# Performance work log

Hardware: AMD Instinct MI355X
Metric: run time of the kernel (lower is better)

The kernel has to match this reference:

```python
import jax, jax.numpy as jnp
import numpy as np

B, N, C = 4, 2048, 1024
H = 16
D = C // H  # head_dim = 64
EPS = 1e-5


def layer_norm(x, g, b):
    mu = jnp.mean(x, axis=-1, keepdims=True)
    var = jnp.var(x, axis=-1, keepdims=True)
    return (x - mu) * jax.lax.rsqrt(var + EPS) * g + b


def setup_inputs() -> dict:
    key = jax.random.key(0)
    ks = jax.random.split(key, 12)
    s = 0.02
    return {
        "x": jax.random.normal(ks[0], (B, N, C), dtype=jnp.float32),
        "Wqkv": jax.random.normal(ks[1], (C, 3 * C), dtype=jnp.float32) * s,
        "bqkv": jnp.zeros((3 * C,), dtype=jnp.float32),
        "Wproj": jax.random.normal(ks[2], (C, C), dtype=jnp.float32) * s,
        "bproj": jnp.zeros((C,), dtype=jnp.float32),
        "g1": jnp.ones((C,), dtype=jnp.float32),
        "b1": jnp.zeros((C,), dtype=jnp.float32),
        "g2": jnp.ones((C,), dtype=jnp.float32),
        "b2": jnp.zeros((C,), dtype=jnp.float32),
        "W1": jax.random.normal(ks[3], (C, 4 * C), dtype=jnp.float32) * s,
        "bf1": jnp.zeros((4 * C,), dtype=jnp.float32),
        "W2": jax.random.normal(ks[4], (4 * C, C), dtype=jnp.float32) * s,
        "bf2": jnp.zeros((C,), dtype=jnp.float32),
    }


def reference(x, Wqkv, bqkv, Wproj, bproj, g1, b1, g2, b2, W1, bf1, W2, bf2):
    # Pre-norm MHA (dropout = identity in eval mode)
    shortcut = x
    h = layer_norm(x, g1, b1)
    qkv = h @ Wqkv + bqkv                       # [B,N,3C]
    qkv = qkv.reshape(B, N, 3, H, D)
    q = jnp.transpose(qkv[:, :, 0], (0, 2, 1, 3))  # [B,H,N,D]
    k = jnp.transpose(qkv[:, :, 1], (0, 2, 1, 3))
    v = jnp.transpose(qkv[:, :, 2], (0, 2, 1, 3))
    scale = D ** -0.5
    attn = jnp.einsum("bhqd,bhkd->bhqk", q, k) * scale
    attn = jax.nn.softmax(attn, axis=-1)
    o = jnp.einsum("bhqk,bhkd->bhqd", attn, v)  # [B,H,N,D]
    o = jnp.transpose(o, (0, 2, 1, 3)).reshape(B, N, C)
    x = o @ Wproj + bproj + shortcut
    # FFN with exact GELU (torch nn.GELU default)
    h2 = layer_norm(x, g2, b2)
    ffn = jax.nn.gelu(h2 @ W1 + bf1, approximate=False) @ W2 + bf2
    return x + ffn
```

## Files before the change

kernel.cpp:

```cpp
#include <hip/hip_runtime.h>
#include <math.h>

using u16 = unsigned short;
typedef __bf16 bf16x8 __attribute__((ext_vector_type(8)));
typedef float f32x4 __attribute__((ext_vector_type(4)));
typedef short s16x4 __attribute__((ext_vector_type(4)));

__device__ __forceinline__ float b2f(u16 u) {
    union { unsigned u; float f; } c; c.u = ((unsigned)u) << 16; return c.f;
}
__device__ __forceinline__ u16 f2b(float f) {
    union { float f; unsigned u; } c; c.f = f;
    return (u16)((c.u + 0x7fffu + ((c.u >> 16) & 1u)) >> 16);
}
__device__ __forceinline__ u16 chop(float f) {
    union { float f; unsigned u; } c; c.f = f;
    return (u16)(c.u >> 16);
}

struct F8 { float v[8]; };
__device__ __forceinline__ F8 unpack8(uint4 r) {
    F8 o;
    o.v[0] = b2f((u16)r.x); o.v[1] = b2f((u16)(r.x >> 16));
    o.v[2] = b2f((u16)r.y); o.v[3] = b2f((u16)(r.y >> 16));
    o.v[4] = b2f((u16)r.z); o.v[5] = b2f((u16)(r.z >> 16));
    o.v[6] = b2f((u16)r.w); o.v[7] = b2f((u16)(r.w >> 16));
    return o;
}

__device__ __forceinline__ void gll16(const void* g, void* l) {
    __builtin_amdgcn_global_load_lds((const __attribute__((address_space(1))) void*)g,
                                     (__attribute__((address_space(3))) void*)l, 16, 0, 0);
}

__global__ __launch_bounds__(256)
void prep_k(const void* __restrict__ s0, const void* __restrict__ s1,
            const void* __restrict__ s2, const void* __restrict__ s3,
            const void* __restrict__ s4, const void* __restrict__ s5,
            const void* __restrict__ s6, const void* __restrict__ s7,
            u16* __restrict__ vec, int* __restrict__ flagp) {
    const u16* gp = (const u16*)s2;
    const int flag = (gp[0] == 0x3F80 && gp[1] == 0x3F80) ? 0 : 1;
    const int i = blockIdx.x * 256 + threadIdx.x;
    if (i == 0) *flagp = flag;
    const void* src; int off;
    if      (i < 3072)  { src = s0; off = 0; }
    else if (i < 4096)  { src = s1; off = 3072; }
    else if (i < 5120)  { src = s2; off = 4096; }
    else if (i < 6144)  { src = s3; off = 5120; }
    else if (i < 7168)  { src = s4; off = 6144; }
    else if (i < 8192)  { src = s5; off = 7168; }
    else if (i < 12288) { src = s6; off = 8192; }
    else                { src = s7; off = 12288; }
    const int j = i - off;
    vec[i] = flag ? f2b(((const float*)src)[j]) : ((const u16*)src)[j];
}

__global__ __launch_bounds__(256)
void transpose_k(const void* __restrict__ src, u16* __restrict__ dst,
                 int R, int Cc, int srcStride, int srcOff, const int* __restrict__ flagp) {
    const int flag = *flagp;
    __shared__ u16 t[32][33];
    const int bx = blockIdx.x * 32;
    const int by = blockIdx.y * 32;
    const int tx = threadIdx.x & 31;
    const int ty = threadIdx.x >> 5;
    if (flag) {
        const float* s = (const float*)src + srcOff;
#pragma unroll
        for (int i = 0; i < 32; i += 8)
            t[ty + i][tx] = f2b(s[(size_t)(by + ty + i) * srcStride + bx + tx]);
    } else {
        const u16* s = (const u16*)src + srcOff;
#pragma unroll
        for (int i = 0; i < 32; i += 8)
            t[ty + i][tx] = s[(size_t)(by + ty + i) * srcStride + bx + tx];
    }
    __syncthreads();
#pragma unroll
    for (int i = 0; i < 32; i += 8)
        dst[(size_t)(bx + ty + i) * R + by + tx] = t[tx][ty + i];
}

__global__ __launch_bounds__(256)
void ln_kernel(const void* __restrict__ x, const u16* __restrict__ g,
               const u16* __restrict__ b, u16* __restrict__ out,
               int srcExt, const int* __restrict__ flagp) {
    const int eff = srcExt ? *flagp : 0;
    const int row = blockIdx.x;
    const int tid = threadIdx.x;
    float v0, v1, v2, v3;
    if (eff) {
        const float4 f = *(const float4*)((const float*)x + (size_t)row * 1024 + tid * 4);
        v0 = f.x; v1 = f.y; v2 = f.z; v3 = f.w;
    } else {
        const uint2 raw = *(const uint2*)((const u16*)x + (size_t)row * 1024 + tid * 4);
        v0 = b2f((u16)raw.x); v1 = b2f((u16)(raw.x >> 16));
        v2 = b2f((u16)raw.y); v3 = b2f((u16)(raw.y >> 16));
    }
    float s  = v0 + v1 + v2 + v3;
    float ss = v0 * v0 + v1 * v1 + v2 * v2 + v3 * v3;
#pragma unroll
    for (int off = 32; off > 0; off >>= 1) {
        s  += __shfl_down(s,  off, 64);
        ss += __shfl_down(ss, off, 64);
    }
    __shared__ float red[8];
    const int wave = tid >> 6, lane = tid & 63;
    if (lane == 0) { red[wave] = s; red[4 + wave] = ss; }
    __syncthreads();
    s  = red[0] + red[1] + red[2] + red[3];
    ss = red[4] + red[5] + red[6] + red[7];
    const float mu  = s * (1.f / 1024.f);
    const float var = ss * (1.f / 1024.f) - mu * mu;
    const float rs  = rsqrtf(var + 1e-5f);
    const int c = tid * 4;
    const uint2 graw = *(const uint2*)(g + c);
    const uint2 braw = *(const uint2*)(b + c);
    u16 o0 = f2b((v0 - mu) * rs * b2f((u16)graw.x)         + b2f((u16)braw.x));
    u16 o1 = f2b((v1 - mu) * rs * b2f((u16)(graw.x >> 16)) + b2f((u16)(braw.x >> 16)));
    u16 o2 = f2b((v2 - mu) * rs * b2f((u16)graw.y)         + b2f((u16)braw.y));
    u16 o3 = f2b((v3 - mu) * rs * b2f((u16)(graw.y >> 16)) + b2f((u16)(braw.y >> 16)));
    uint2 w; w.x = (unsigned)o0 | ((unsigned)o1 << 16); w.y = (unsigned)o2 | ((unsigned)o3 << 16);
    *(uint2*)(out + (size_t)row * 1024 + c) = w;
}

template<int ACT, bool ACCUM, bool RES_EXT>
__global__ __launch_bounds__(256)
void gemm_bt(const u16* __restrict__ A, const u16* __restrict__ Bt,
             const u16* __restrict__ bias, const void* __restrict__ res,
             u16* __restrict__ C, int M, int K, int ldc, const int* __restrict__ flagp) {
    const int flag = RES_EXT ? *flagp : 0;
    __shared__ u16 As[128 * 32];
    __shared__ u16 Bs[128 * 32];
    const int tid  = threadIdx.x;
    const int lane = tid & 63;
    const int wave = tid >> 6;
    const int wr   = (wave >> 1) * 64;
    const int wc   = (wave & 1) * 64;
    const int lr   = lane & 15;
    const int quad = lane >> 4;
    const int bm = blockIdx.x * 128;
    const int bn = blockIdx.y * 128;
    const int scol = (tid & 3) * 8;
    const int srow = tid >> 2;

    f32x4 acc[4][4] = {};

    const u16* Arow0 = A  + (size_t)(bm + srow) * K + scol;
    const u16* Arow1 = A  + (size_t)(bm + 64 + srow) * K + scol;
    const u16* Brow0 = Bt + (size_t)(bn + srow) * K + scol;
    const u16* Brow1 = Bt + (size_t)(bn + 64 + srow) * K + scol;

    u16* asd0 = &As[wave * 512];
    u16* asd1 = &As[2048 + wave * 512];
    u16* bsd0 = &Bs[wave * 512];
    u16* bsd1 = &Bs[2048 + wave * 512];

    for (int k0 = 0; k0 < K; k0 += 32) {
        gll16(Arow0 + k0, asd0);
        gll16(Arow1 + k0, asd1);
        gll16(Brow0 + k0, bsd0);
        gll16(Brow1 + k0, bsd1);
        __syncthreads();
        bf16x8 af[4], bfr[4];
#pragma unroll
        for (int i = 0; i < 4; ++i)
            af[i] = *(const bf16x8*)(&As[(wr + i * 16 + lr) * 32 + quad * 8]);
#pragma unroll
        for (int j = 0; j < 4; ++j)
            bfr[j] = *(const bf16x8*)(&Bs[(wc + j * 16 + lr) * 32 + quad * 8]);
#pragma unroll
        for (int i = 0; i < 4; ++i)
#pragma unroll
            for (int j = 0; j < 4; ++j)
                acc[i][j] = __builtin_amdgcn_mfma_f32_16x16x32_bf16(af[i], bfr[j], acc[i][j], 0, 0, 0);
        __syncthreads();
    }

#pragma unroll
    for (int i = 0; i < 4; ++i) {
#pragma unroll
        for (int j = 0; j < 4; ++j) {
#pragma unroll
            for (int r = 0; r < 4; ++r) {
                const int row = bm + wr + i * 16 + quad * 4 + r;
                const int col = bn + wc + j * 16 + lr;
                const size_t idx = (size_t)row * ldc + col;
                float v = acc[i][j][r];
                if (bias) v += b2f(bias[col]);
                if (ACT == 1) v = 0.5f * v * (1.0f + erff(v * 0.70710678118654752f));
                if (res) {
                    if (RES_EXT && flag) v += ((const float*)res)[idx];
                    else                 v += b2f(((const u16*)res)[idx]);
                }
                if (ACCUM) v += b2f(C[idx]);
                C[idx] = f2b(v);
            }
        }
    }
}

__device__ __forceinline__ void stage4(const u16* __restrict__ A,
        const u16* __restrict__ Bt, char* lds, int bm, int bn, int K,
        int t, int ty, int tid) {
    const int k0   = t << 6;
    const int bufo = (t & 1) << 16;
    const u16* src;
    int rowbase, base;
    if (ty < 2) { src = A;  rowbase = bm + ty * 128;       base = bufo + ty * 16384; }
    else        { src = Bt; rowbase = bn + (ty - 2) * 128; base = bufo + 32768 + (ty - 2) * 16384; }
#pragma unroll
    for (int i = 0; i < 2; ++i) {
        const int w    = tid * 16 + i * 8192;
        const int row  = w >> 7;
        const int colB = (w & 127) ^ ((row & 7) << 4);
        const u16* g = src + (size_t)(rowbase + row) * K + k0 + (colB >> 1);
        char* d = lds + base + ((tid >> 6) << 10) + i * 8192;
        gll16(g, d);
    }
}
__device__ __forceinline__ void stage3(const u16* __restrict__ A,
        const u16* __restrict__ Bt, char* lds, int bm, int bn, int K,
        int t, int ty, int tid) {
    const int k0   = t << 6;
    const int bufo = (t & 1) * 49152;
    const u16* src;
    int rowbase, base;
    if (ty < 2) { src = A;  rowbase = bm + ty * 128; base = bufo + ty * 16384; }
    else        { src = Bt; rowbase = bn;            base = bufo + 32768; }
#pragma unroll
    for (int i = 0; i < 2; ++i) {
        const int w    = tid * 16 + i * 8192;
        const int row  = w >> 7;
        const int colB = (w & 127) ^ ((row & 7) << 4);
        const u16* g = src + (size_t)(rowbase + row) * K + k0 + (colB >> 1);
        char* d = lds + base + ((tid >> 6) << 10) + i * 8192;
        gll16(g, d);
    }
}

template<int ACT, bool RES_EXT>
__global__ __launch_bounds__(512, 2)
void gemm256(const u16* __restrict__ A, const u16* __restrict__ Bt,
             const u16* __restrict__ bias, const void* __restrict__ res,
             u16* __restrict__ C, int nbx, int K, int ldc,
             const int* __restrict__ flagp) {
    extern __shared__ char lds[];
    const int flag = RES_EXT ? *flagp : 0;

    const int nwg = gridDim.x;
    const int q8  = nwg >> 3;
    const int bid = blockIdx.x;
    const int swz = (bid & 7) * q8 + (bid >> 3);
    const int bm  = (swz % nbx) * 256;
    const int bn  = (swz / nbx) * 256;

    const int tid  = threadIdx.x;
    const int lane = tid & 63, wave = tid >> 6;
    const int lr   = lane & 15, quad = lane >> 4;
    const int wm   = wave >> 2, wn = wave & 3;

    const int nt    = K >> 6;
    const int niter = nt >> 1;

    stage4(A, Bt, lds, bm, bn, K, 0, 0, tid);
    stage4(A, Bt, lds, bm, bn, K, 0, 2, tid);
    stage4(A, Bt, lds, bm, bn, K, 0, 1, tid);
    stage4(A, Bt, lds, bm, bn, K, 0, 3, tid);
    stage4(A, Bt, lds, bm, bn, K, 1, 0, tid);
    stage4(A, Bt, lds, bm, bn, K, 1, 2, tid);
    stage4(A, Bt, lds, bm, bn, K, 1, 1, tid);
    asm volatile("s_waitcnt vmcnt(6)" ::: "memory");
    __builtin_amdgcn_s_barrier();

    f32x4 acc[8][4] = {};
    const int cq = quad * 16;

    for (int it = 0; it < niter; ++it) {
        const bool lastpair = (it == niter - 1);
#pragma unroll
        for (int hf = 0; hf < 2; ++hf) {
            const int T    = 2 * it + hf;
            const int bufo = (T & 1) << 16;
            bf16x8 a0[4][2], a1[4][2], b0[2][2], b1[2][2];

#pragma unroll
            for (int m = 0; m < 4; ++m) {
                const int rA = wm * 64 + m * 16 + lr;
                const int sw = (rA & 7) << 4;
#pragma unroll
                for (int ks = 0; ks < 2; ++ks)
                    a0[m][ks] = *(const bf16x8*)(lds + bufo + rA * 128 + ((ks * 64 + cq) ^ sw));
            }
#pragma unroll
            for (int n = 0; n < 2; ++n) {
                const int rB = wn * 32 + n * 16 + lr;
                const int sw = (rB & 7) << 4;
#pragma unroll
                for (int ks = 0; ks < 2; ++ks)
                    b0[n][ks] = *(const bf16x8*)(lds + bufo + 32768 + rB * 128 + ((ks * 64 + cq) ^ sw));
            }
            if (T + 1 < nt) stage4(A, Bt, lds, bm, bn, K, T + 1, 3, tid);
            __builtin_amdgcn_s_barrier();
            asm volatile("s_waitcnt lgkmcnt(0)" ::: "memory");
            __builtin_amdgcn_s_setprio(1);
#pragma unroll
            for (int m = 0; m < 4; ++m)
#pragma unroll
                for (int n = 0; n < 2; ++n) {
                    acc[m][n] = __builtin_amdgcn_mfma_f32_16x16x32_bf16(a0[m][0], b0[n][0], acc[m][n], 0, 0, 0);
                    acc[m][n] = __builtin_amdgcn_mfma_f32_16x16x32_bf16(a0[m][1], b0[n][1], acc[m][n], 0, 0, 0);
                }
            __builtin_amdgcn_s_setprio(0);
            __builtin_amdgcn_s_barrier();

#pragma unroll
            for (int n = 0; n < 2; ++n) {
                const int rB = wn * 32 + n * 16 + lr;
                const int sw = (rB & 7) << 4;
#pragma unroll
                for (int ks = 0; ks < 2; ++ks)
                    b1[n][ks] = *(const bf16x8*)(lds + bufo + 49152 + rB * 128 + ((ks * 64 + cq) ^ sw));
            }
            if (T + 2 < nt) stage4(A, Bt, lds, bm, bn, K, T + 2, 0, tid);
            __builtin_amdgcn_s_barrier();
            asm volatile("s_waitcnt lgkmcnt(0)" ::: "memory");
            __builtin_amdgcn_s_setprio(1);
#pragma unroll
            for (int m = 0; m < 4; ++m)
#pragma unroll
                for (int n = 0; n < 2; ++n) {
                    acc[m][2 + n] = __builtin_amdgcn_mfma_f32_16x16x32_bf16(a0[m][0], b1[n][0], acc[m][2 + n], 0, 0, 0);
                    acc[m][2 + n] = __builtin_amdgcn_mfma_f32_16x16x32_bf16(a0[m][1], b1[n][1], acc[m][2 + n], 0, 0, 0);
                }
            __builtin_amdgcn_s_setprio(0);
            __builtin_amdgcn_s_barrier();

#pragma unroll
            for (int m = 0; m < 4; ++m) {
                const int rA = wm * 64 + m * 16 + lr;
                const int sw = (rA & 7) << 4;
#pragma unroll
                for (int ks = 0; ks < 2; ++ks)
                    a1[m][ks] = *(const bf16x8*)(lds + bufo + 16384 + rA * 128 + ((ks * 64 + cq) ^ sw));
            }
            if (T + 2 < nt) stage4(A, Bt, lds, bm, bn, K, T + 2, 2, tid);
            __builtin_amdgcn_s_barrier();
            asm volatile("s_waitcnt lgkmcnt(0)" ::: "memory");
            __builtin_amdgcn_s_setprio(1);
#pragma unroll
            for (int m = 0; m < 4; ++m)
#pragma unroll
                for (int n = 0; n < 2; ++n) {
                    acc[4 + m][n] = __builtin_amdgcn_mfma_f32_16x16x32_bf16(a1[m][0], b0[n][0], acc[4 + m][n], 0, 0, 0);
                    acc[4 + m][n] = __builtin_amdgcn_mfma_f32_16x16x32_bf16(a1[m][1], b0[n][1], acc[4 + m][n], 0, 0, 0);
                }
            __builtin_amdgcn_s_setprio(0);
            __builtin_amdgcn_s_barrier();

            if (T + 2 < nt) stage4(A, Bt, lds, bm, bn, K, T + 2, 1, tid);
            if (lastpair) asm volatile("s_waitcnt vmcnt(0)" ::: "memory");
            else          asm volatile("s_waitcnt vmcnt(6)" ::: "memory");
            __builtin_amdgcn_s_barrier();
            __builtin_amdgcn_s_setprio(1);
#pragma unroll
            for (int m = 0; m < 4; ++m)
#pragma unroll
                for (int n = 0; n < 2; ++n) {
                    acc[4 + m][2 + n] = __builtin_amdgcn_mfma_f32_16x16x32_bf16(a1[m][0], b1[n][0], acc[4 + m][2 + n], 0, 0, 0);
                    acc[4 + m][2 + n] = __builtin_amdgcn_mfma_f32_16x16x32_bf16(a1[m][1], b1[n][1], acc[4 + m][2 + n], 0, 0, 0);
                }
            __builtin_amdgcn_s_setprio(0);
            __builtin_amdgcn_s_barrier();
        }
    }

#pragma unroll
    for (int mi = 0; mi < 8; ++mi) {
        const int row = bm + (mi >> 2) * 128 + wm * 64 + (mi & 3) * 16 + quad * 4;
#pragma unroll
        for (int nj = 0; nj < 4; ++nj) {
            const int col = bn + (nj >> 1) * 128 + wn * 32 + (nj & 1) * 16 + lr;
            const float bia = bias ? b2f(bias[col]) : 0.f;
#pragma unroll
            for (int r = 0; r < 4; ++r) {
                const size_t idx = (size_t)(row + r) * ldc + col;
                float v = acc[mi][nj][r] + bia;
                if (ACT == 1) v = 0.5f * v * (1.0f + erff(v * 0.70710678118654752f));
                if (res) {
                    if (RES_EXT && flag) v += ((const float*)res)[idx];
                    else                 v += b2f(((const u16*)res)[idx]);
                }
                C[idx] = f2b(v);
            }
        }
    }
}

template<int ACT, bool RES_EXT, int OUTM>
__global__ __launch_bounds__(512, 2)
void gemm256n(const u16* __restrict__ A, const u16* __restrict__ Bt,
              const u16* __restrict__ bias, const void* __restrict__ res,
              u16* __restrict__ C, void* __restrict__ outF, int nbx, int K, int ldc,
              const int* __restrict__ flagp) {
    extern __shared__ char lds[];
    const int flag = (RES_EXT || OUTM) ? *flagp : 0;

    const int nwg = gridDim.x;
    const int q8  = nwg >> 3;
    const int bid = blockIdx.x;
    const int swz = (bid & 7) * q8 + (bid >> 3);
    const int bm  = (swz % nbx) * 256;
    const int bn  = (swz / nbx) * 128;

    const int tid  = threadIdx.x;
    const int lane = tid & 63, wave = tid >> 6;
    const int lr   = lane & 15, quad = lane >> 4;
    const int wm   = wave >> 2, wn = wave & 3;

    const int nt = K >> 6;

    stage3(A, Bt, lds, bm, bn, K, 0, 0, tid);
    stage3(A, Bt, lds, bm, bn, K, 0, 2, tid);
    stage3(A, Bt, lds, bm, bn, K, 0, 1, tid);
    stage3(A, Bt, lds, bm, bn, K, 1, 0, tid);
    stage3(A, Bt, lds, bm, bn, K, 1, 2, tid);
    stage3(A, Bt, lds, bm, bn, K, 1, 1, tid);
    asm volatile("s_waitcnt vmcnt(6)" ::: "memory");
    __builtin_amdgcn_s_barrier();

    f32x4 acc[8][2] = {};
    const int cq = quad * 16;

    for (int T = 0; T < nt; ++T) {
        const int bufo = (T & 1) * 49152;
        bf16x8 a0[4][2], a1[4][2], b[2][2];

#pragma unroll
        for (int m = 0; m < 4; ++m) {
            const int rA = wm * 64 + m * 16 + lr;
            const int sw = (rA & 7) << 4;
#pragma unroll
            for (int ks = 0; ks < 2; ++ks)
                a0[m][ks] = *(const bf16x8*)(lds + bufo + rA * 128 + ((ks * 64 + cq) ^ sw));
        }
#pragma unroll
        for (int n = 0; n < 2; ++n) {
            const int rB = wn * 32 + n * 16 + lr;
            const int sw = (rB & 7) << 4;
#pragma unroll
            for (int ks = 0; ks < 2; ++ks)
                b[n][ks] = *(const bf16x8*)(lds + bufo + 32768 + rB * 128 + ((ks * 64 + cq) ^ sw));
        }
        __builtin_amdgcn_s_barrier();
        asm volatile("s_waitcnt lgkmcnt(0)" ::: "memory");
        __builtin_amdgcn_s_setprio(1);
#pragma unroll
        for (int m = 0; m < 4; ++m)
#pragma unroll
            for (int n = 0; n < 2; ++n) {
                acc[m][n] = __builtin_amdgcn_mfma_f32_16x16x32_bf16(a0[m][0], b[n][0], acc[m][n], 0, 0, 0);
                acc[m][n] = __builtin_amdgcn_mfma_f32_16x16x32_bf16(a0[m][1], b[n][1], acc[m][n], 0, 0, 0);
            }
        __builtin_amdgcn_s_setprio(0);
        __builtin_amdgcn_s_barrier();

#pragma unroll
        for (int m = 0; m < 4; ++m) {
            const int rA = wm * 64 + m * 16 + lr;
            const int sw = (rA & 7) << 4;
#pragma unroll
            for (int ks = 0; ks < 2; ++ks)
                a1[m][ks] = *(const bf16x8*)(lds + bufo + 16384 + rA * 128 + ((ks * 64 + cq) ^ sw));
        }
        if (T + 2 < nt) {
            stage3(A, Bt, lds, bm, bn, K, T + 2, 0, tid);
            stage3(A, Bt, lds, bm, bn, K, T + 2, 2, tid);
        }
        __builtin_amdgcn_s_barrier();
        asm volatile("s_waitcnt lgkmcnt(0)" ::: "memory");
        __builtin_amdgcn_s_setprio(1);
#pragma unroll
        for (int m = 0; m < 4; ++m)
#pragma unroll
            for (int n = 0; n < 2; ++n) {
                acc[4 + m][n] = __builtin_amdgcn_mfma_f32_16x16x32_bf16(a1[m][0], b[n][0], acc[4 + m][n], 0, 0, 0);
                acc[4 + m][n] = __builtin_amdgcn_mfma_f32_16x16x32_bf16(a1[m][1], b[n][1], acc[4 + m][n], 0, 0, 0);
            }
        __builtin_amdgcn_s_setprio(0);
        __builtin_amdgcn_s_barrier();
        if (T + 2 < nt) stage3(A, Bt, lds, bm, bn, K, T + 2, 1, tid);
        if (T >= nt - 2) asm volatile("s_waitcnt vmcnt(0)" ::: "memory");
        else             asm volatile("s_waitcnt vmcnt(6)" ::: "memory");
        __builtin_amdgcn_s_barrier();
    }

#pragma unroll
    for (int mi = 0; mi < 8; ++mi) {
        const int row = bm + (mi >> 2) * 128 + wm * 64 + (mi & 3) * 16 + quad * 4;
#pragma unroll
        for (int nj = 0; nj < 2; ++nj) {
            const int col = bn + wn * 32 + nj * 16 + lr;
            const float bia = bias ? b2f(bias[col]) : 0.f;
#pragma unroll
            for (int r = 0; r < 4; ++r) {
                const size_t idx = (size_t)(row + r) * ldc + col;
                float v = acc[mi][nj][r] + bia;
                if (ACT == 1) v = 0.5f * v * (1.0f + erff(v * 0.70710678118654752f));
                if (res) {
                    if (RES_EXT && flag) v += ((const float*)res)[idx];
                    else                 v += b2f(((const u16*)res)[idx]);
                }
                if (OUTM) {
                    if (flag) ((float*)outF)[idx] = v;
                    else      ((u16*)outF)[idx]  = f2b(v);
                } else {
                    C[idx] = f2b(v);
                }
            }
        }
    }
}

__global__ __launch_bounds__(512)
void flash_attn(const u16* __restrict__ qkv, u16* __restrict__ o) {
    const int bid = blockIdx.x;
    const int s   = bid >> 3;
    const int bh  = (bid & 7) * 8 + (s & 7);
    const int qt  = s >> 3;
    const int b = bh >> 4, h = bh & 15;
    const int qbase = qt * 256;

    __shared__ u16 smem[25600];

    const int tid  = threadIdx.x;
    const int lane = tid & 63;
    const int wave = tid >> 6;
    const int lr   = lane & 15;
    const int quad = lane >> 4;
    const int wq   = wave * 32;

    const u16* base = qkv + (size_t)b * 2048 * 3072 + h * 64;

    const int kst = tid & 63;
    const int d8  = tid >> 6;
    const u16* ksrc0 = base + 1024 + (size_t)kst * 3072 + d8 * 8;
    const u16* vsrc0 = base + 2048 + (size_t)kst * 3072 + d8 * 8;

    {
        const int row = tid & 255, seg = tid >> 8;
        const u16* src = base + (size_t)(qbase + row) * 3072 + seg * 32;
        const int sw = (row >> 2) & 3;
        u16* dstrow = &smem[9216 + row * 64];
#pragma unroll
        for (int j = 0; j < 4; ++j) {
            F8 f = unpack8(*(const uint4*)(src + j * 8));
            u16 t[8];
#pragma unroll
            for (int e = 0; e < 8; ++e) t[e] = f2b(f.v[e] * 0.18033688011112042f);
            uint4 w;
            w.x = (unsigned)t[0] | ((unsigned)t[1] << 16);
            w.y = (unsigned)t[2] | ((unsigned)t[3] << 16);
            w.z = (unsigned)t[4] | ((unsigned)t[5] << 16);
            w.w = (unsigned)t[6] | ((unsigned)t[7] << 16);
            const int grp = seg * 2 + (j >> 1);
            *(uint4*)(dstrow + ((grp ^ sw) * 16 + (j & 1) * 8)) = w;
        }
        uint4 k0 = *(const uint4*)(ksrc0);
        uint4 v0 = *(const uint4*)(vsrc0);
        *(uint4*)(&smem[kst * 72 + d8 * 8]) = k0;
        u16 vv[8];
        *(uint4*)(vv) = v0;
#pragma unroll
        for (int j = 0; j < 8; ++j)
            smem[4608 + (d8 * 8 + j) * 72 + kst] = vv[j];
    }
    __syncthreads();

    bf16x8 qf[2][2];
#pragma unroll
    for (int mi = 0; mi < 2; ++mi)
#pragma unroll
        for (int ks = 0; ks < 2; ++ks) {
            const int row = wq + mi * 16 + lr;
            const int phys = (ks * 2 + (quad >> 1)) ^ ((lr >> 2) & 3);
            qf[mi][ks] = *(const bf16x8*)(&smem[9216 + row * 64 + phys * 16 + (quad & 1) * 8]);
        }
    __syncthreads();

    f32x4 OT[2][4] = {};
    float lp[2] = { 0.f, 0.f };

    for (int kt = 0; kt < 32; ++kt) {
        const int cb = (kt & 1) * 9216;
        const int nb = 9216 - cb;
        uint4 nk0, nv0;
        if (kt < 31) {
            const size_t off = (size_t)(kt + 1) * 64 * 3072;
            nk0 = *(const uint4*)(ksrc0 + off);
            nv0 = *(const uint4*)(vsrc0 + off);
        }

        bf16x8 kf[4][2];
#pragma unroll
        for (int t = 0; t < 4; ++t)
#pragma unroll
            for (int ks = 0; ks < 2; ++ks)
                kf[t][ks] = *(const bf16x8*)(&smem[cb + (t * 16 + lr) * 72 + ks * 32 + quad * 8]);
        f32x4 st[4][2];
#pragma unroll
        for (int t = 0; t < 4; ++t)
#pragma unroll
            for (int mi = 0; mi < 2; ++mi) {
                f32x4 z = { 0.f, 0.f, 0.f, 0.f };
                z = __builtin_amdgcn_mfma_f32_16x16x32_bf16(kf[t][0], qf[mi][0], z, 0, 0, 0);
                st[t][mi] = __builtin_amdgcn_mfma_f32_16x16x32_bf16(kf[t][1], qf[mi][1], z, 0, 0, 0);
            }

        s16x4 pf[4][2];
#pragma unroll
        for (int t = 0; t < 4; ++t)
#pragma unroll
            for (int mi = 0; mi < 2; ++mi) {
                const float e0 = exp2f(st[t][mi][0]);
                const float e1 = exp2f(st[t][mi][1]);
                const float e2 = exp2f(st[t][mi][2]);
                const float e3 = exp2f(st[t][mi][3]);
                lp[mi] += (e0 + e1) + (e2 + e3);
                s16x4 p;
                p[0] = (short)chop(e0); p[1] = (short)chop(e1);
                p[2] = (short)chop(e2); p[3] = (short)chop(e3);
                pf[t][mi] = p;
            }

#pragma unroll
        for (int dj = 0; dj < 4; ++dj)
#pragma unroll
            for (int t = 0; t < 4; ++t) {
                const s16x4 vf = *(const s16x4*)(&smem[cb + 4608 + (dj * 16 + lr) * 72 + t * 16 + quad * 4]);
                OT[0][dj] = __builtin_amdgcn_mfma_f32_16x16x16bf16_1k(vf, pf[t][0], OT[0][dj], 0, 0, 0);
                OT[1][dj] = __builtin_amdgcn_mfma_f32_16x16x16bf16_1k(vf, pf[t][1], OT[1][dj], 0, 0, 0);
            }

        if (kt < 31) {
            *(uint4*)(&smem[nb + kst * 72 + d8 * 8]) = nk0;
            u16 vv[8];
            *(uint4*)(vv) = nv0;
#pragma unroll
            for (int j = 0; j < 8; ++j)
                smem[nb + 4608 + (d8 * 8 + j) * 72 + kst] = vv[j];
        }
        __syncthreads();
    }

#pragma unroll
    for (int mi = 0; mi < 2; ++mi) {
        float l = lp[mi];
        l += __shfl_xor(l, 16);
        l += __shfl_xor(l, 32);
        lp[mi] = 1.f / l;
    }
#pragma unroll
    for (int mi = 0; mi < 2; ++mi) {
        const float inv = lp[mi];
        const int row = qbase + wq + mi * 16 + lr;
        u16* orow = o + (size_t)(b * 2048 + row) * 1024 + h * 64;
#pragma unroll
        for (int dj = 0; dj < 4; ++dj) {
            const u16 a0 = f2b(OT[mi][dj][0] * inv);
            const u16 a1 = f2b(OT[mi][dj][1] * inv);
            const u16 a2 = f2b(OT[mi][dj][2] * inv);
            const u16 a3 = f2b(OT[mi][dj][3] * inv);
            uint2 w;
            w.x = (unsigned)a0 | ((unsigned)a1 << 16);
            w.y = (unsigned)a2 | ((unsigned)a3 << 16);
            *(uint2*)(orow + dj * 16 + quad * 4) = w;
        }
    }
}

__global__ __launch_bounds__(256)
void store_out(const u16* __restrict__ src, void* __restrict__ dst, int n,
               const int* __restrict__ flagp) {
    const int flag = *flagp;
    const int base = (blockIdx.x * 256 + threadIdx.x) * 8;
    if (base >= n) return;
    const uint4 r = *(const uint4*)(src + base);
    if (flag) {
        F8 f = unpack8(r);
        float4* d = (float4*)((float*)dst + base);
        d[0] = make_float4(f.v[0], f.v[1], f.v[2], f.v[3]);
        d[1] = make_float4(f.v[4], f.v[5], f.v[6], f.v[7]);
    } else {
        *(uint4*)((u16*)dst + base) = r;
    }
}

extern "C" void kernel_launch(void* const* d_in, const int* in_sizes, int n_in,
                              void* d_out, int out_size, void* d_ws, size_t ws_size,
                              hipStream_t stream) {
    const void* x     = d_in[0];
    const void* Wqkv  = d_in[1];
    const void* bqkv  = d_in[2];
    const void* Wproj = d_in[3];
    const void* bproj = d_in[4];
    const void* g1    = d_in[5];
    const void* b1    = d_in[6];
    const void* g2    = d_in[7];
    const void* b2    = d_in[8];
    const void* W1    = d_in[9];
    const void* bf1   = d_in[10];
    const void* W2    = d_in[11];
    const void* bf2   = d_in[12];

    char* ws = (char*)d_ws;
    int* flagp = (int*)ws;
    u16* vec  = (u16*)(ws + 256);
    u16* vbqkv = vec,        *vbproj = vec + 3072;
    u16* vg1 = vec + 4096,   *vb1 = vec + 5120;
    u16* vg2 = vec + 6144,   *vb2 = vec + 7168;
    u16* vbf1 = vec + 8192,  *vbf2 = vec + 12288;
    u16* lno = (u16*)d_out;

    static bool ldsInit = false;
    if (!ldsInit) {
        hipFuncSetAttribute((const void*)gemm256<1, false>,
                            hipFuncAttributeMaxDynamicSharedMemorySize, 131072);
        hipFuncSetAttribute((const void*)gemm256n<0, false, 0>,
                            hipFuncAttributeMaxDynamicSharedMemorySize, 98304);
        hipFuncSetAttribute((const void*)gemm256n<0, true, 0>,
                            hipFuncAttributeMaxDynamicSharedMemorySize, 98304);
        hipFuncSetAttribute((const void*)gemm256n<0, false, 1>,
                            hipFuncAttributeMaxDynamicSharedMemorySize, 98304);
        ldsInit = true;
    }

    prep_k<<<52, 256, 0, stream>>>(bqkv, bproj, g1, b1, g2, b2, bf1, bf2, vec, flagp);

    if (ws_size >= 127000000ull) {
        u16* wT   = (u16*)(ws + 65536);
        u16* QKV  = (u16*)(ws + 9437184);
        u16* x2   = QKV;
        u16* h2   = (u16*)(ws + 26214400);
        u16* F1   = (u16*)(ws + 59768832);
        u16* ACC  = F1;

        ln_kernel<<<8192, 256, 0, stream>>>(x, vg1, vb1, lno, 1, flagp);
        transpose_k<<<dim3(96, 32), 256, 0, stream>>>(Wqkv, wT, 1024, 3072, 3072, 0, flagp);
        gemm256n<0, false, 0><<<dim3(768), 512, 98304, stream>>>(
            lno, wT, vbqkv, nullptr, QKV, nullptr, 32, 1024, 3072, flagp);
        flash_attn<<<dim3(512), 512, 0, stream>>>(QKV, ACC);
        transpose_k<<<dim3(32, 32), 256, 0, stream>>>(Wproj, wT, 1024, 1024, 1024, 0, flagp);
        gemm256n<0, true, 0><<<dim3(256), 512, 98304, stream>>>(
            ACC, wT, vbproj, x, x2, nullptr, 32, 1024, 1024, flagp);
        ln_kernel<<<8192, 256, 0, stream>>>(x2, vg2, vb2, h2, 0, flagp);
        transpose_k<<<dim3(128, 32), 256, 0, stream>>>(W1, wT, 1024, 4096, 4096, 0, flagp);
        gemm256<1, false><<<dim3(512), 512, 131072, stream>>>(
            h2, wT, vbf1, nullptr, F1, 32, 1024, 4096, flagp);
        transpose_k<<<dim3(32, 128), 256, 0, stream>>>(W2, wT, 4096, 1024, 1024, 0, flagp);
        gemm256n<0, false, 1><<<dim3(256), 512, 98304, stream>>>(
            F1, wT, vbf2, x2, nullptr, d_out, 32, 4096, 1024, flagp);
    } else {
        u16* wT  = (u16*)(ws + 65536);
        u16* BIG = (u16*)(ws + 4194304);
        u16* x2  = BIG;
        u16* h2  = (u16*)(ws + 4194304 + 16777216);
        u16* f1c = (u16*)(ws + 4194304 + 33554432);
        u16* ACC = (u16*)(ws + 54525952);

        ln_kernel<<<8192, 256, 0, stream>>>(x, vg1, vb1, lno, 1, flagp);
        for (int s = 0; s < 3; ++s) {
            transpose_k<<<dim3(32, 32), 256, 0, stream>>>(Wqkv, wT, 1024, 1024, 3072, s * 1024, flagp);
            gemm_bt<0, false, false><<<dim3(64, 8), 256, 0, stream>>>(
                lno, wT, vbqkv + s * 1024, nullptr, BIG + s * 1024, 8192, 1024, 3072, flagp);
        }
        flash_attn<<<dim3(512), 512, 0, stream>>>(BIG, ACC);
        transpose_k<<<dim3(32, 32), 256, 0, stream>>>(Wproj, wT, 1024, 1024, 1024, 0, flagp);
        gemm_bt<0, false, true><<<dim3(64, 8), 256, 0, stream>>>(
            ACC, wT, vbproj, x, x2, 8192, 1024, 1024, flagp);
        ln_kernel<<<8192, 256, 0, stream>>>(x2, vg2, vb2, h2, 0, flagp);
        for (int c = 0; c < 4; ++c) {
            transpose_k<<<dim3(32, 32), 256, 0, stream>>>(W1, wT, 1024, 1024, 4096, c * 1024, flagp);
            gemm_bt<1, false, false><<<dim3(64, 8), 256, 0, stream>>>(
                h2, wT, vbf1 + c * 1024, nullptr, f1c, 8192, 1024, 1024, flagp);
            transpose_k<<<dim3(32, 32), 256, 0, stream>>>(W2, wT, 1024, 1024, 1024, c * 1024 * 1024, flagp);
            if (c == 0)
                gemm_bt<0, false, false><<<dim3(64, 8), 256, 0, stream>>>(
                    f1c, wT, vbf2, nullptr, ACC, 8192, 1024, 1024, flagp);
            else if (c < 3)
                gemm_bt<0, true, false><<<dim3(64, 8), 256, 0, stream>>>(
                    f1c, wT, nullptr, nullptr, ACC, 8192, 1024, 1024, flagp);
            else
                gemm_bt<0, true, false><<<dim3(64, 8), 256, 0, stream>>>(
                    f1c, wT, nullptr, x2, ACC, 8192, 1024, 1024, flagp);
        }
        store_out<<<4096, 256, 0, stream>>>(ACC, d_out, 8388608, flagp);
    }
}
```

Measured before the change: 602.6 us.

## Write V transposed from QKV GEMM epilogue so attention loads V with vector stores

The QKV GEMM epilogue now writes the V columns in a transposed per-head layout [B*H, D, N] into a separate workspace buffer, packing four rows per 8-byte store. Flash attention gains a template path that reads this transposed V and writes it to LDS with one 16-byte store per thread. This replaces the eight scalar 2-byte transposing LDS stores per tile. The aim is to cut LDS store traffic and bank conflicts in the attention inner loop, at the cost of a strided global write pattern for V in the GEMM epilogue and an extra workspace region.

```diff
diff --git a/kernel.cpp b/kernel.cpp
--- a/kernel.cpp
+++ b/kernel.cpp
@@ -405,7 +405,7 @@
               u16* __restrict__ C, void* __restrict__ outF, int nbx, int K, int ldc,
               const int* __restrict__ flagp) {
     extern __shared__ char lds[];
-    const int flag = (RES_EXT || OUTM) ? *flagp : 0;
+    const int flag = (RES_EXT || OUTM == 1) ? *flagp : 0;
 
     const int nwg = gridDim.x;
     const int q8  = nwg >> 3;
@@ -496,6 +496,28 @@
         __builtin_amdgcn_s_barrier();
     }
 
+    if (OUTM == 2 && bn >= 2048) {
+#pragma unroll
+        for (int mi = 0; mi < 8; ++mi) {
+            const int row = bm + (mi >> 2) * 128 + wm * 64 + (mi & 3) * 16 + quad * 4;
+            const int bb = row >> 11, n = row & 2047;
+#pragma unroll
+            for (int nj = 0; nj < 2; ++nj) {
+                const int col = bn + wn * 32 + nj * 16 + lr;
+                const float bia = bias ? b2f(bias[col]) : 0.f;
+                u16 q0 = f2b(acc[mi][nj][0] + bia);
+                u16 q1 = f2b(acc[mi][nj][1] + bia);
+                u16 q2 = f2b(acc[mi][nj][2] + bia);
+                u16 q3 = f2b(acc[mi][nj][3] + bia);
+                uint2 w;
+                w.x = (unsigned)q0 | ((unsigned)q1 << 16);
+                w.y = (unsigned)q2 | ((unsigned)q3 << 16);
+                *(uint2*)((u16*)outF + (((size_t)(bb * 1024 + col - 2048)) << 11) + n) = w;
+            }
+        }
+        return;
+    }
+
 #pragma unroll
     for (int mi = 0; mi < 8; ++mi) {
         const int row = bm + (mi >> 2) * 128 + wm * 64 + (mi & 3) * 16 + quad * 4;
@@ -512,7 +534,7 @@
                     if (RES_EXT && flag) v += ((const float*)res)[idx];
                     else                 v += b2f(((const u16*)res)[idx]);
                 }
-                if (OUTM) {
+                if (OUTM == 1) {
                     if (flag) ((float*)outF)[idx] = v;
                     else      ((u16*)outF)[idx]  = f2b(v);
                 } else {
@@ -523,8 +545,10 @@
     }
 }
 
+template<int USEVT>
 __global__ __launch_bounds__(512)
-void flash_attn(const u16* __restrict__ qkv, u16* __restrict__ o) {
+void flash_attn(const u16* __restrict__ qkv, const u16* __restrict__ vt,
+                u16* __restrict__ o) {
     const int bid = blockIdx.x;
     const int s   = bid >> 3;
     const int bh  = (bid & 7) * 8 + (s & 7);
@@ -546,7 +570,15 @@
     const int kst = tid & 63;
     const int d8  = tid >> 6;
     const u16* ksrc0 = base + 1024 + (size_t)kst * 3072 + d8 * 8;
-    const u16* vsrc0 = base + 2048 + (size_t)kst * 3072 + d8 * 8;
+    const u16* vsrc0;
+    int vlds;
+    if (USEVT) {
+        vsrc0 = vt + ((size_t)bh * 64 + kst) * 2048 + d8 * 8;
+        vlds  = kst * 72 + d8 * 8;
+    } else {
+        vsrc0 = base + 2048 + (size_t)kst * 3072 + d8 * 8;
+        vlds  = 0;
+    }
 
     {
         const int row = tid & 255, seg = tid >> 8;
@@ -570,11 +602,15 @@
         uint4 k0 = *(const uint4*)(ksrc0);
         uint4 v0 = *(const uint4*)(vsrc0);
         *(uint4*)(&smem[kst * 72 + d8 * 8]) = k0;
-        u16 vv[8];
-        *(uint4*)(vv) = v0;
-#pragma unroll
-        for (int j = 0; j < 8; ++j)
-            smem[4608 + (d8 * 8 + j) * 72 + kst] = vv[j];
+        if (USEVT) {
+            *(uint4*)(&smem[4608 + vlds]) = v0;
+        } else {
+            u16 vv[8];
+            *(uint4*)(vv) = v0;
+#pragma unroll
+            for (int j = 0; j < 8; ++j)
+                smem[4608 + (d8 * 8 + j) * 72 + kst] = vv[j];
+        }
     }
     __syncthreads();
 
@@ -597,9 +633,9 @@
         const int nb = 9216 - cb;
         uint4 nk0, nv0;
         if (kt < 31) {
-            const size_t off = (size_t)(kt + 1) * 64 * 3072;
-            nk0 = *(const uint4*)(ksrc0 + off);
-            nv0 = *(const uint4*)(vsrc0 + off);
+            nk0 = *(const uint4*)(ksrc0 + (size_t)(kt + 1) * 64 * 3072);
+            nv0 = USEVT ? *(const uint4*)(vsrc0 + (size_t)(kt + 1) * 64)
+                        : *(const uint4*)(vsrc0 + (size_t)(kt + 1) * 64 * 3072);
         }
 
         bf16x8 kf[4][2];
@@ -645,11 +681,15 @@
 
         if (kt < 31) {
             *(uint4*)(&smem[nb + kst * 72 + d8 * 8]) = nk0;
-            u16 vv[8];
-            *(uint4*)(vv) = nv0;
-#pragma unroll
-            for (int j = 0; j < 8; ++j)
-                smem[nb + 4608 + (d8 * 8 + j) * 72 + kst] = vv[j];
+            if (USEVT) {
+                *(uint4*)(&smem[nb + 4608 + vlds]) = nv0;
+            } else {
+                u16 vv[8];
+                *(uint4*)(vv) = nv0;
+#pragma unroll
+                for (int j = 0; j < 8; ++j)
+                    smem[nb + 4608 + (d8 * 8 + j) * 72 + kst] = vv[j];
+            }
         }
         __syncthreads();
     }
@@ -727,7 +767,7 @@
     if (!ldsInit) {
         hipFuncSetAttribute((const void*)gemm256<1, false>,
                             hipFuncAttributeMaxDynamicSharedMemorySize, 131072);
-        hipFuncSetAttribute((const void*)gemm256n<0, false, 0>,
+        hipFuncSetAttribute((const void*)gemm256n<0, false, 2>,
                             hipFuncAttributeMaxDynamicSharedMemorySize, 98304);
         hipFuncSetAttribute((const void*)gemm256n<0, true, 0>,
                             hipFuncAttributeMaxDynamicSharedMemorySize, 98304);
@@ -743,14 +783,15 @@
         u16* QKV  = (u16*)(ws + 9437184);
         u16* x2   = QKV;
         u16* h2   = (u16*)(ws + 26214400);
+        u16* VT   = (u16*)(ws + 42991616);
         u16* F1   = (u16*)(ws + 59768832);
         u16* ACC  = F1;
 
         ln_kernel<<<8192, 256, 0, stream>>>(x, vg1, vb1, lno, 1, flagp);
         transpose_k<<<dim3(96, 32), 256, 0, stream>>>(Wqkv, wT, 1024, 3072, 3072, 0, flagp);
-        gemm256n<0, false, 0><<<dim3(768), 512, 98304, stream>>>(
-            lno, wT, vbqkv, nullptr, QKV, nullptr, 32, 1024, 3072, flagp);
-        flash_attn<<<dim3(512), 512, 0, stream>>>(QKV, ACC);
+        gemm256n<0, false, 2><<<dim3(768), 512, 98304, stream>>>(
+            lno, wT, vbqkv, nullptr, QKV, VT, 32, 1024, 3072, flagp);
+        flash_attn<1><<<dim3(512), 512, 0, stream>>>(QKV, VT, ACC);
         transpose_k<<<dim3(32, 32), 256, 0, stream>>>(Wproj, wT, 1024, 1024, 1024, 0, flagp);
         gemm256n<0, true, 0><<<dim3(256), 512, 98304, stream>>>(
             ACC, wT, vbproj, x, x2, nullptr, 32, 1024, 1024, flagp);
@@ -775,7 +816,7 @@
             gemm_bt<0, false, false><<<dim3(64, 8), 256, 0, stream>>>(
                 lno, wT, vbqkv + s * 1024, nullptr, BIG + s * 1024, 8192, 1024, 3072, flagp);
         }
-        flash_attn<<<dim3(512), 512, 0, stream>>>(BIG, ACC);
+        flash_attn<0><<<dim3(512), 512, 0, stream>>>(BIG, nullptr, ACC);
         transpose_k<<<dim3(32, 32), 256, 0, stream>>>(Wproj, wT, 1024, 1024, 1024, 0, flagp);
         gemm_bt<0, false, true><<<dim3(64, 8), 256, 0, stream>>>(
             ACC, wT, vbproj, x, x2, 8192, 1024, 1024, flagp);
```

Result: no change. 596.5 us (-1.0%).
